# Kernel optimization log

Hardware: AMD Instinct MI355X
Metric: run time of the kernel (lower is better)

The kernel has to match this reference:

```python
import jax, jax.numpy as jnp
import numpy as np

S, N, MSA_DIM, PAIR_DIM, D, H = 8, 256, 256, 128, 32, 8
EPS = 1e-5


def layer_norm(x, w, b):
    mu = jnp.mean(x, axis=-1, keepdims=True)
    var = jnp.mean((x - mu) ** 2, axis=-1, keepdims=True)
    return (x - mu) * jax.lax.rsqrt(var + EPS) * w + b


def setup_inputs() -> dict:
    key = jax.random.key(0)
    ks = jax.random.split(key, 8)
    def rnd(k, shape, scale=1.0):
        return jax.random.normal(k, shape, jnp.float32) * scale
    return {
        "msa_rep": rnd(ks[0], (S, N, MSA_DIM)),
        "pair_rep": rnd(ks[1], (N, N, PAIR_DIM)),
        "ln_w": jnp.ones((MSA_DIM,), jnp.float32),
        "ln_b": jnp.zeros((MSA_DIM,), jnp.float32),
        "w_qkv": rnd(ks[2], (MSA_DIM, 3 * H * D), 0.02),
        "ln_pair_w": jnp.ones((PAIR_DIM,), jnp.float32),
        "ln_pair_b": jnp.zeros((PAIR_DIM,), jnp.float32),
        "w_b": rnd(ks[3], (PAIR_DIM, H), 0.02),
        "w_g": rnd(ks[4], (MSA_DIM, H * D), 0.02),
        "w_out": rnd(ks[5], (H * D, MSA_DIM), 0.02),
        "b_out": jnp.zeros((MSA_DIM,), jnp.float32),
    }


def reference(msa_rep, pair_rep, ln_w, ln_b, w_qkv, ln_pair_w, ln_pair_b,
              w_b, w_g, w_out, b_out):
    s, n, _ = msa_rep.shape
    x = layer_norm(msa_rep, ln_w, ln_b)                      # [s, n, msa_dim]
    qkv = x @ w_qkv                                          # [s, n, 3*h*d]
    # chunk(3, dim=-1) then view(..., d, h): d outer, h inner
    q, k, v = [t.reshape(s, n, D, H) for t in jnp.split(qkv, 3, axis=-1)]
    # pair bias: LN + linear -> [n, n, h], broadcast to [1, i, j, 1, h]
    b = layer_norm(pair_rep, ln_pair_w, ln_pair_b) @ w_b     # [n, n, h]
    g = jax.nn.sigmoid(x @ w_g).reshape(s, n, D, H)          # gate [s, n, d, h]
    # NOTE: logits keep the d axis (no contraction): einsum 'sidh,sjdh->sijdh'
    scores = (q[:, :, None, :, :] * k[:, None, :, :, :]) * (D ** -0.5) \
             + b[None, :, :, None, :]                        # [s, i, j, d, h]
    a = jax.nn.softmax(scores, axis=2)                       # softmax over j
    out = g * jnp.einsum('sijdh,sjdh->sidh', a, v)           # [s, n, d, h]
    return out.reshape(s, n, D * H) @ w_out + b_out          # [s, n, msa_dim]
```

## Files before the change

kernel.cpp:

```cpp
#include <hip/hip_runtime.h>
#include <math.h>

#define S_DIM 8
#define N_RES 256
#define MSA_DIM 256
#define PAIR_DIM 128
#define D_DIM 32
#define H_DIM 8
#define M_ROWS (S_DIM * N_RES)
#define QKV_N (3 * H_DIM * D_DIM)
#define HD (H_DIM * D_DIM)
#define XW_N 1024
#define LOG2E 1.4426950408889634f

typedef __attribute__((ext_vector_type(8))) short short8;
typedef __attribute__((ext_vector_type(4))) float floatx4;

#define DPP_ADD(x, ctrl, rmask)                                                \
    x += __int_as_float(__builtin_amdgcn_update_dpp(                           \
        0, __float_as_int(x), (ctrl), (rmask), 0xf, true))

__device__ __forceinline__ float wave_sum63(float x) {
    DPP_ADD(x, 0x111, 0xf);
    DPP_ADD(x, 0x112, 0xf);
    DPP_ADD(x, 0x114, 0xf);
    DPP_ADD(x, 0x118, 0xf);
    DPP_ADD(x, 0x142, 0xa);
    DPP_ADD(x, 0x143, 0xc);
    return x;
}

__device__ __forceinline__ float quad_sum(float x) {
    x += __int_as_float(__builtin_amdgcn_update_dpp(
        0, __float_as_int(x), 0xB1, 0xf, 0xf, true));
    x += __int_as_float(__builtin_amdgcn_update_dpp(
        0, __float_as_int(x), 0x4E, 0xf, 0xf, true));
    return x;
}

__device__ __forceinline__ unsigned short bf16rn(float v) {
    unsigned u = __float_as_uint(v);
    return (unsigned short)((u + 0x7FFF + ((u >> 16) & 1)) >> 16);
}

__global__ __launch_bounds__(256) void prep_kernel(
    const float* __restrict__ pair, const float* __restrict__ lw,
    const float* __restrict__ lb, const float* __restrict__ wb,
    float* __restrict__ b2,
    const float* __restrict__ w_qkv, const float* __restrict__ w_g,
    unsigned short* __restrict__ whiT, unsigned short* __restrict__ wloT,
    const float* __restrict__ w_out,
    unsigned short* __restrict__ wouthiT, unsigned short* __restrict__ woutloT,
    const float* __restrict__ msa, const float* __restrict__ lnw,
    const float* __restrict__ lnb, unsigned short* __restrict__ xhi,
    unsigned short* __restrict__ xlo)
{
    __shared__ __align__(16) float shm[2080];
    int bx = blockIdx.x;
    int t = threadIdx.x;

    if (bx < 1024) {
        float* As = shm;
        float* Spart = shm + 1552;
        float* Qpart = shm + 1816;
        if (t < 128) {
            float lwc = lw[t];
#pragma unroll
            for (int h = 0; h < 8; h++)
                As[t * 12 + h] = lwc * wb[t * 8 + h] * LOG2E;
        }
        __syncthreads();
        {
            int h = t >> 5, seg = t & 31, cbase = seg * 4;
            float sa = 0, sq = 0;
#pragma unroll
            for (int cc = 0; cc < 4; cc++) {
                int c = cbase + cc;
                sa += As[c * 12 + h];
                sq += lb[c] * wb[c * 8 + h];
            }
            Spart[h * 33 + seg] = sa;
            Qpart[h * 33 + seg] = sq * LOG2E;
        }
        __syncthreads();
        if (t < 8) {
            float s = 0, q = 0;
#pragma unroll
            for (int j = 0; j < 32; j++) {
                s += Spart[t * 33 + j];
                q += Qpart[t * 33 + j];
            }
            As[1536 + t] = s;
            As[1544 + t] = q;
        }
        __syncthreads();
        int row = bx * 64 + (t >> 2);
        int q = t & 3;
        const float* in = pair + (size_t)row * PAIR_DIM;
        float4 x4[8];
#pragma unroll
        for (int it = 0; it < 8; it++)
            x4[it] = *(const float4*)&in[it * 16 + q * 4];
        float s = 0, s2 = 0;
        float dot[8] = {};
#pragma unroll
        for (int it = 0; it < 8; it++) {
            float xk[4];
            *(float4*)xk = x4[it];
#pragma unroll
            for (int k = 0; k < 4; k++) {
                int c = it * 16 + q * 4 + k;
                float xv = xk[k];
                s += xv; s2 += xv * xv;
                float4 A0 = *(const float4*)&As[c * 12];
                float4 A1 = *(const float4*)&As[c * 12 + 4];
                dot[0] += xv * A0.x; dot[1] += xv * A0.y;
                dot[2] += xv * A0.z; dot[3] += xv * A0.w;
                dot[4] += xv * A1.x; dot[5] += xv * A1.y;
                dot[6] += xv * A1.z; dot[7] += xv * A1.w;
            }
        }
        s = quad_sum(s);
        s2 = quad_sum(s2);
#pragma unroll
        for (int h = 0; h < 8; h++) dot[h] = quad_sum(dot[h]);
        float mu = s * (1.0f / 128.0f);
        float var = s2 * (1.0f / 128.0f) - mu * mu;
        float rs = rsqrtf(var + 1e-5f);
        int h0 = q * 2;
#pragma unroll
        for (int u = 0; u < 2; u++) {
            int h = h0 + u;
            b2[h * 65536 + row] = rs * (dot[h] - mu * As[1536 + h]) + As[1544 + h];
        }
    } else if (bx < 1152) {
        int id = (bx - 1024) * 256 + t;
        int n = id >> 5, oct = id & 31, k0 = oct * 8;
        const float* src;
        int stride;
        if (n < QKV_N) { src = w_qkv + n; stride = QKV_N; }
        else           { src = w_g + (n - QKV_N); stride = HD; }
        unsigned short h8[8], l8[8];
#pragma unroll
        for (int j = 0; j < 8; j++) {
            float v = src[(size_t)(k0 + j) * stride];
            unsigned short h = bf16rn(v);
            h8[j] = h;
            l8[j] = bf16rn(v - __uint_as_float((unsigned)h << 16));
        }
        *(short8*)&whiT[n * 256 + k0] = *(short8*)h8;
        *(short8*)&wloT[n * 256 + k0] = *(short8*)l8;
    } else if (bx < 1184) {
        int id = (bx - 1152) * 256 + t;
        int n = id >> 5, oct = id & 31, k0 = oct * 8;
        unsigned short h8[8], l8[8];
#pragma unroll
        for (int j = 0; j < 8; j++) {
            int k = k0 + j;
            int wrow = (k & 31) * 8 + (k >> 5);
            float v = w_out[(size_t)wrow * 256 + n];
            unsigned short h = bf16rn(v);
            h8[j] = h;
            l8[j] = bf16rn(v - __uint_as_float((unsigned)h << 16));
        }
        *(short8*)&wouthiT[n * 256 + k0] = *(short8*)h8;
        *(short8*)&woutloT[n * 256 + k0] = *(short8*)l8;
    } else {
        int row = bx - 1184;
        float v = msa[row * MSA_DIM + t];
        float s1 = wave_sum63(v);
        float s2 = wave_sum63(v * v);
        float* r1 = shm;
        float* r2 = shm + 4;
        int wave = t >> 6, lane = t & 63;
        if (lane == 63) { r1[wave] = s1; r2[wave] = s2; }
        __syncthreads();
        float S1 = r1[0] + r1[1] + r1[2] + r1[3];
        float S2 = r2[0] + r2[1] + r2[2] + r2[3];
        float mu = S1 * (1.0f / 256.0f);
        float var = S2 * (1.0f / 256.0f) - mu * mu;
        float rs = rsqrtf(var + 1e-5f);
        float y = (v - mu) * rs * lnw[t] + lnb[t];
        unsigned short h = bf16rn(y);
        xhi[row * 256 + t] = h;
        xlo[row * 256 + t] = bf16rn(y - __uint_as_float((unsigned)h << 16));
    }
}

__global__ __launch_bounds__(256) void xw_mfma_kernel(
    const unsigned short* __restrict__ xhi, const unsigned short* __restrict__ xlo,
    const unsigned short* __restrict__ whiT, const unsigned short* __restrict__ wloT,
    float* __restrict__ q_t, float* __restrict__ k_t,
    float* __restrict__ v_t, float* __restrict__ g_t)
{
    __shared__ unsigned short As[64 * 72];
    __shared__ unsigned short Bs[128 * 72];
    __shared__ float Cs[64 * 132];
    int t = threadIdx.x;
    int n0 = blockIdx.x * 128, m0 = blockIdx.y * 64;
    int w = t >> 6, L = t & 63;
    int wm = (w & 1) * 32, wn = (w >> 1) * 64;
    int l15 = L & 15, l4 = L >> 4;
    int alm = t >> 3, alk = (t & 7) * 8;
    floatx4 acc[2][4];
#pragma unroll
    for (int a = 0; a < 2; a++)
#pragma unroll
        for (int b = 0; b < 4; b++) acc[a][b] = (floatx4){0, 0, 0, 0};

    short8 pa0 = *(const short8*)&xhi[(m0 + alm) * 256 + alk];
    short8 pa1 = *(const short8*)&xhi[(m0 + alm + 32) * 256 + alk];
    short8 pb[4];
#pragma unroll
    for (int j = 0; j < 4; j++) {
        int id = t + 256 * j;
        int bn = id >> 3, bc = (id & 7) * 8;
        pb[j] = *(const short8*)&whiT[(n0 + bn) * 256 + bc];
    }

    for (int r = 0; r < 12; r++) {
        __syncthreads();
        *(short8*)&As[alm * 72 + alk] = pa0;
        *(short8*)&As[(alm + 32) * 72 + alk] = pa1;
#pragma unroll
        for (int j = 0; j < 4; j++) {
            int id = t + 256 * j;
            int bn = id >> 3, bc = (id & 7) * 8;
            *(short8*)&Bs[bn * 72 + bc] = pb[j];
        }
        __syncthreads();
        if (r < 11) {
            int rn = r + 1;
            int seg = rn >> 2, kb = (rn & 3) * 64;
            const unsigned short* An = (seg == 1) ? xlo : xhi;
            const unsigned short* Bn = (seg == 2) ? wloT : whiT;
            pa0 = *(const short8*)&An[(m0 + alm) * 256 + kb + alk];
            pa1 = *(const short8*)&An[(m0 + alm + 32) * 256 + kb + alk];
#pragma unroll
            for (int j = 0; j < 4; j++) {
                int id = t + 256 * j;
                int bn = id >> 3, bc = (id & 7) * 8;
                pb[j] = *(const short8*)&Bn[(n0 + bn) * 256 + kb + bc];
            }
        }
#pragma unroll
        for (int ks = 0; ks < 2; ks++) {
            int ko = ks * 32 + l4 * 8;
            short8 af[2], bf[4];
#pragma unroll
            for (int a = 0; a < 2; a++)
                af[a] = *(short8*)&As[(wm + a * 16 + l15) * 72 + ko];
#pragma unroll
            for (int b = 0; b < 4; b++)
                bf[b] = *(short8*)&Bs[(wn + b * 16 + l15) * 72 + ko];
#pragma unroll
            for (int a = 0; a < 2; a++)
#pragma unroll
                for (int b = 0; b < 4; b++)
                    acc[a][b] = __builtin_amdgcn_mfma_f32_16x16x32_bf16(
                        af[a], bf[b], acc[a][b], 0, 0, 0);
        }
    }
#pragma unroll
    for (int a = 0; a < 2; a++)
#pragma unroll
        for (int b = 0; b < 4; b++) {
            int nl = wn + b * 16 + l15;
#pragma unroll
            for (int rg = 0; rg < 4; rg++) {
                int ml = wm + a * 16 + l4 * 4 + rg;
                Cs[ml * 132 + nl] = acc[a][b][rg];
            }
        }
    __syncthreads();
    int qkv_mode = (n0 < QKV_N);
    int chunk = n0 >> 8;
    int dbase = (n0 & 255) >> 3;
#pragma unroll
    for (int j = 0; j < 8; j++) {
        int id = t + 256 * j;
        int m = id >> 5;
        int h = (id >> 2) & 7;
        int dq = id & 3;
        float vals[4];
#pragma unroll
        for (int jj = 0; jj < 4; jj++)
            vals[jj] = Cs[m * 132 + (dq * 4 + jj) * 8 + h];
        int mm = m0 + m;
        int daddr = dbase + dq * 4;
        if (qkv_mode) {
            float* dst = (chunk == 0) ? q_t : ((chunk == 1) ? k_t : v_t);
            *(float4*)&dst[(size_t)(h * M_ROWS + mm) * D_DIM + daddr] =
                *(float4*)vals;
        } else {
            float4 o;
            o.x = 1.0f / (1.0f + __expf(-vals[0]));
            o.y = 1.0f / (1.0f + __expf(-vals[1]));
            o.z = 1.0f / (1.0f + __expf(-vals[2]));
            o.w = 1.0f / (1.0f + __expf(-vals[3]));
            *(float4*)&g_t[(size_t)(h * M_ROWS + mm) * D_DIM + daddr] = o;
        }
    }
}

__global__ __launch_bounds__(256) void attn_kernel(
    const float* __restrict__ q_t, const float* __restrict__ k_t,
    const float* __restrict__ v_t, const float* __restrict__ g_t,
    const float* __restrict__ b2, unsigned short* __restrict__ ao_hi,
    unsigned short* __restrict__ ao_lo)
{
    __shared__ float k_sh[256][32];
    __shared__ float v_sh[256][32];
    int blk = blockIdx.x;
    int h = blk & 7, s = (blk >> 3) & 7, it = blk >> 6;
    int t = threadIdx.x;
    const float* kb = k_t + (size_t)(h * M_ROWS + s * N_RES) * D_DIM;
    const float* vb = v_t + (size_t)(h * M_ROWS + s * N_RES) * D_DIM;
    for (int idx = t; idx < 2048; idx += 256) {
        ((float4*)k_sh)[idx] = ((const float4*)kb)[idx];
        ((float4*)v_sh)[idx] = ((const float4*)vb)[idx];
    }
    __syncthreads();
    int jp = t & 3, dg = (t >> 2) & 7, li = t >> 5;
    int d0 = dg * 4;
    const float SCL2 = 0.17677669529663687f * LOG2E;
    int ig[4], mrow[4];
    float qs[4][4];
#pragma unroll
    for (int r = 0; r < 4; r++) {
        ig[r] = it * 32 + r * 8 + li;
        mrow[r] = s * N_RES + ig[r];
        float4 q4 = *(const float4*)&q_t[(size_t)(h * M_ROWS + mrow[r]) * D_DIM + d0];
        qs[r][0] = q4.x * SCL2; qs[r][1] = q4.y * SCL2;
        qs[r][2] = q4.z * SCL2; qs[r][3] = q4.w * SCL2;
    }
    float den[4][4] = {}, acc[4][4] = {};
    const float* bbase = b2 + h * 65536;
    for (int js4 = 0; js4 < 16; js4++) {
        float bb[4][4];
#pragma unroll
        for (int r = 0; r < 4; r++)
            *(float4*)&bb[r][0] =
                *(const float4*)&bbase[ig[r] * 256 + jp * 64 + js4 * 4];
#pragma unroll
        for (int u = 0; u < 4; u++) {
            int j = jp * 64 + js4 * 4 + u;
            float ka[4], va[4];
            *(float4*)ka = *(const float4*)&k_sh[j][d0];
            *(float4*)va = *(const float4*)&v_sh[j][d0];
#pragma unroll
            for (int r = 0; r < 4; r++) {
#pragma unroll
                for (int c = 0; c < 4; c++) {
                    float e = __builtin_amdgcn_exp2f(qs[r][c] * ka[c] + bb[r][u]);
                    den[r][c] += e;
                    acc[r][c] += e * va[c];
                }
            }
        }
    }
#pragma unroll
    for (int r = 0; r < 4; r++)
#pragma unroll
        for (int c = 0; c < 4; c++) {
            den[r][c] = quad_sum(den[r][c]);
            acc[r][c] = quad_sum(acc[r][c]);
        }
    if (jp == 0) {
#pragma unroll
        for (int r = 0; r < 4; r++) {
            float4 g4 = *(const float4*)&g_t[(size_t)(h * M_ROWS + mrow[r]) * D_DIM + d0];
            float o[4];
            o[0] = g4.x * acc[r][0] / den[r][0];
            o[1] = g4.y * acc[r][1] / den[r][1];
            o[2] = g4.z * acc[r][2] / den[r][2];
            o[3] = g4.w * acc[r][3] / den[r][3];
            unsigned short hi[4], lo[4];
#pragma unroll
            for (int c = 0; c < 4; c++) {
                hi[c] = bf16rn(o[c]);
                lo[c] = bf16rn(o[c] - __uint_as_float((unsigned)hi[c] << 16));
            }
            size_t base = (size_t)mrow[r] * 256 + h * 32 + d0;
            uint2 ph, pl;
            ph.x = (unsigned)hi[0] | ((unsigned)hi[1] << 16);
            ph.y = (unsigned)hi[2] | ((unsigned)hi[3] << 16);
            pl.x = (unsigned)lo[0] | ((unsigned)lo[1] << 16);
            pl.y = (unsigned)lo[2] | ((unsigned)lo[3] << 16);
            *(uint2*)&ao_hi[base] = ph;
            *(uint2*)&ao_lo[base] = pl;
        }
    }
}

__global__ __launch_bounds__(256) void out_mfma_kernel(
    const unsigned short* __restrict__ ahi, const unsigned short* __restrict__ alo,
    const unsigned short* __restrict__ whi, const unsigned short* __restrict__ wlo,
    const float* __restrict__ bias, float* __restrict__ out)
{
    __shared__ unsigned short As[64 * 72];
    __shared__ unsigned short Bs[128 * 72];
    __shared__ float Cs[64 * 132];
    int t = threadIdx.x;
    int n0 = blockIdx.x * 128, m0 = blockIdx.y * 64;
    int w = t >> 6, L = t & 63;
    int wm = (w & 1) * 32, wn = (w >> 1) * 64;
    int l15 = L & 15, l4 = L >> 4;
    int alm = t >> 3, alk = (t & 7) * 8;
    floatx4 acc[2][4];
#pragma unroll
    for (int a = 0; a < 2; a++)
#pragma unroll
        for (int b = 0; b < 4; b++) acc[a][b] = (floatx4){0, 0, 0, 0};

    short8 pa0 = *(const short8*)&ahi[(m0 + alm) * 256 + alk];
    short8 pa1 = *(const short8*)&ahi[(m0 + alm + 32) * 256 + alk];
    short8 pb[4];
#pragma unroll
    for (int j = 0; j < 4; j++) {
        int id = t + 256 * j;
        int bn = id >> 3, bc = (id & 7) * 8;
        pb[j] = *(const short8*)&whi[(n0 + bn) * 256 + bc];
    }

    for (int r = 0; r < 12; r++) {
        __syncthreads();
        *(short8*)&As[alm * 72 + alk] = pa0;
        *(short8*)&As[(alm + 32) * 72 + alk] = pa1;
#pragma unroll
        for (int j = 0; j < 4; j++) {
            int id = t + 256 * j;
            int bn = id >> 3, bc = (id & 7) * 8;
            *(short8*)&Bs[bn * 72 + bc] = pb[j];
        }
        __syncthreads();
        if (r < 11) {
            int rn = r + 1;
            int seg = rn >> 2, kb = (rn & 3) * 64;
            const unsigned short* An = (seg == 1) ? alo : ahi;
            const unsigned short* Bn = (seg == 2) ? wlo : whi;
            pa0 = *(const short8*)&An[(m0 + alm) * 256 + kb + alk];
            pa1 = *(const short8*)&An[(m0 + alm + 32) * 256 + kb + alk];
#pragma unroll
            for (int j = 0; j < 4; j++) {
                int id = t + 256 * j;
                int bn = id >> 3, bc = (id & 7) * 8;
                pb[j] = *(const short8*)&Bn[(n0 + bn) * 256 + kb + bc];
            }
        }
#pragma unroll
        for (int ks = 0; ks < 2; ks++) {
            int ko = ks * 32 + l4 * 8;
            short8 af[2], bf[4];
#pragma unroll
            for (int a = 0; a < 2; a++)
                af[a] = *(short8*)&As[(wm + a * 16 + l15) * 72 + ko];
#pragma unroll
            for (int b = 0; b < 4; b++)
                bf[b] = *(short8*)&Bs[(wn + b * 16 + l15) * 72 + ko];
#pragma unroll
            for (int a = 0; a < 2; a++)
#pragma unroll
                for (int b = 0; b < 4; b++)
                    acc[a][b] = __builtin_amdgcn_mfma_f32_16x16x32_bf16(
                        af[a], bf[b], acc[a][b], 0, 0, 0);
        }
    }
#pragma unroll
    for (int a = 0; a < 2; a++)
#pragma unroll
        for (int b = 0; b < 4; b++) {
            int nl = wn + b * 16 + l15;
#pragma unroll
            for (int rg = 0; rg < 4; rg++) {
                int ml = wm + a * 16 + l4 * 4 + rg;
                Cs[ml * 132 + nl] = acc[a][b][rg];
            }
        }
    __syncthreads();
#pragma unroll
    for (int j = 0; j < 8; j++) {
        int id = t + 256 * j;
        int m = id >> 5, nc = (id & 31) * 4;
        float4 v = *(float4*)&Cs[m * 132 + nc];
        float4 bb = *(const float4*)&bias[n0 + nc];
        float4 o;
        o.x = v.x + bb.x; o.y = v.y + bb.y;
        o.z = v.z + bb.z; o.w = v.w + bb.w;
        *(float4*)&out[(size_t)(m0 + m) * 256 + n0 + nc] = o;
    }
}

extern "C" void kernel_launch(void* const* d_in, const int* in_sizes, int n_in,
                              void* d_out, int out_size, void* d_ws, size_t ws_size,
                              hipStream_t stream)
{
    const float* msa_rep   = (const float*)d_in[0];
    const float* pair_rep  = (const float*)d_in[1];
    const float* ln_w      = (const float*)d_in[2];
    const float* ln_b      = (const float*)d_in[3];
    const float* w_qkv     = (const float*)d_in[4];
    const float* ln_pair_w = (const float*)d_in[5];
    const float* ln_pair_b = (const float*)d_in[6];
    const float* w_b       = (const float*)d_in[7];
    const float* w_g       = (const float*)d_in[8];
    const float* w_out     = (const float*)d_in[9];
    const float* b_out     = (const float*)d_in[10];
    float* out = (float*)d_out;

    float* ws = (float*)d_ws;
    const size_t CH = 524288;
    float* q_t = ws + 0 * CH;
    float* k_t = ws + 1 * CH;
    float* v_t = ws + 2 * CH;
    float* g_t = ws + 3 * CH;
    float* b2  = ws + 4 * CH;
    unsigned short* ao_hi   = (unsigned short*)(ws + 5 * CH);
    unsigned short* ao_lo   = ao_hi + (size_t)M_ROWS * 256;
    unsigned short* xhi     = (unsigned short*)(ws + 6 * CH);
    unsigned short* xlo     = xhi + (size_t)M_ROWS * 256;
    unsigned short* whiT    = (unsigned short*)(ws + 7 * CH);
    unsigned short* wloT    = whiT + (size_t)XW_N * 256;
    unsigned short* wouthiT = (unsigned short*)(ws + 8 * CH);
    unsigned short* woutloT = wouthiT + 65536;

    prep_kernel<<<3232, 256, 0, stream>>>(
        pair_rep, ln_pair_w, ln_pair_b, w_b, b2,
        w_qkv, w_g, whiT, wloT,
        w_out, wouthiT, woutloT,
        msa_rep, ln_w, ln_b, xhi, xlo);

    xw_mfma_kernel<<<dim3(8, 32), 256, 0, stream>>>(
        xhi, xlo, whiT, wloT, q_t, k_t, v_t, g_t);

    attn_kernel<<<512, 256, 0, stream>>>(q_t, k_t, v_t, g_t, b2, ao_hi, ao_lo);

    out_mfma_kernel<<<dim3(2, 32), 256, 0, stream>>>(
        ao_hi, ao_lo, wouthiT, woutloT, b_out, out);
}
```

Baseline: 144.3 us.

## Move pair-bias LN into a fused mid kernel alongside smaller-tile QKV GEMM

Pair-bias layernorm/projection moves out of the prep kernel into a new mid kernel. There it runs interleaved (2 of every 3 blocks) with the QKV/gate GEMM, now tiled 64x64 so that more blocks cover the GPU. The output GEMM tiles shrink to 32x64 to raise the block count from 64 to 256. Attention K/V shared arrays get a padded stride of 40 to reduce LDS bank conflicts. Smaller tiles reload more operand data, and the mixed-role kernel has to allocate the larger shared-memory footprint for every block.

```diff
diff --git a/kernel.cpp b/kernel.cpp
--- a/kernel.cpp
+++ b/kernel.cpp
@@ -44,9 +44,6 @@
 }
 
 __global__ __launch_bounds__(256) void prep_kernel(
-    const float* __restrict__ pair, const float* __restrict__ lw,
-    const float* __restrict__ lb, const float* __restrict__ wb,
-    float* __restrict__ b2,
     const float* __restrict__ w_qkv, const float* __restrict__ w_g,
     unsigned short* __restrict__ whiT, unsigned short* __restrict__ wloT,
     const float* __restrict__ w_out,
@@ -55,14 +52,83 @@
     const float* __restrict__ lnb, unsigned short* __restrict__ xhi,
     unsigned short* __restrict__ xlo)
 {
-    __shared__ __align__(16) float shm[2080];
+    __shared__ float shm[8];
     int bx = blockIdx.x;
     int t = threadIdx.x;
 
-    if (bx < 1024) {
-        float* As = shm;
-        float* Spart = shm + 1552;
-        float* Qpart = shm + 1816;
+    if (bx < 2048) {
+        int row = bx;
+        float v = msa[row * MSA_DIM + t];
+        float s1 = wave_sum63(v);
+        float s2 = wave_sum63(v * v);
+        float* r1 = shm;
+        float* r2 = shm + 4;
+        int wave = t >> 6, lane = t & 63;
+        if (lane == 63) { r1[wave] = s1; r2[wave] = s2; }
+        __syncthreads();
+        float S1 = r1[0] + r1[1] + r1[2] + r1[3];
+        float S2 = r2[0] + r2[1] + r2[2] + r2[3];
+        float mu = S1 * (1.0f / 256.0f);
+        float var = S2 * (1.0f / 256.0f) - mu * mu;
+        float rs = rsqrtf(var + 1e-5f);
+        float y = (v - mu) * rs * lnw[t] + lnb[t];
+        unsigned short h = bf16rn(y);
+        xhi[row * 256 + t] = h;
+        xlo[row * 256 + t] = bf16rn(y - __uint_as_float((unsigned)h << 16));
+    } else if (bx < 2176) {
+        int id = (bx - 2048) * 256 + t;
+        int n = id >> 5, oct = id & 31, k0 = oct * 8;
+        const float* src;
+        int stride;
+        if (n < QKV_N) { src = w_qkv + n; stride = QKV_N; }
+        else           { src = w_g + (n - QKV_N); stride = HD; }
+        unsigned short h8[8], l8[8];
+#pragma unroll
+        for (int j = 0; j < 8; j++) {
+            float v = src[(size_t)(k0 + j) * stride];
+            unsigned short h = bf16rn(v);
+            h8[j] = h;
+            l8[j] = bf16rn(v - __uint_as_float((unsigned)h << 16));
+        }
+        *(short8*)&whiT[n * 256 + k0] = *(short8*)h8;
+        *(short8*)&wloT[n * 256 + k0] = *(short8*)l8;
+    } else {
+        int id = (bx - 2176) * 256 + t;
+        int n = id >> 5, oct = id & 31, k0 = oct * 8;
+        unsigned short h8[8], l8[8];
+#pragma unroll
+        for (int j = 0; j < 8; j++) {
+            int k = k0 + j;
+            int wrow = (k & 31) * 8 + (k >> 5);
+            float v = w_out[(size_t)wrow * 256 + n];
+            unsigned short h = bf16rn(v);
+            h8[j] = h;
+            l8[j] = bf16rn(v - __uint_as_float((unsigned)h << 16));
+        }
+        *(short8*)&wouthiT[n * 256 + k0] = *(short8*)h8;
+        *(short8*)&woutloT[n * 256 + k0] = *(short8*)l8;
+    }
+}
+
+__global__ __launch_bounds__(256) void mid_kernel(
+    const float* __restrict__ pair, const float* __restrict__ lw,
+    const float* __restrict__ lb, const float* __restrict__ wb,
+    float* __restrict__ b2,
+    const unsigned short* __restrict__ xhi, const unsigned short* __restrict__ xlo,
+    const unsigned short* __restrict__ whiT, const unsigned short* __restrict__ wloT,
+    float* __restrict__ q_t, float* __restrict__ k_t,
+    float* __restrict__ v_t, float* __restrict__ g_t)
+{
+    __shared__ __align__(16) char smem[35840];
+    int bx = blockIdx.x;
+    int t = threadIdx.x;
+    int g3 = bx / 3, r3 = bx - g3 * 3;
+
+    if (r3 != 2) {
+        float* As = (float*)smem;
+        float* Spart = (float*)smem + 1552;
+        float* Qpart = (float*)smem + 1816;
+        int pair_id = g3 * 2 + r3;
         if (t < 128) {
             float lwc = lw[t];
 #pragma unroll
@@ -94,7 +160,7 @@
             As[1544 + t] = q;
         }
         __syncthreads();
-        int row = bx * 64 + (t >> 2);
+        int row = pair_id * 64 + (t >> 2);
         int q = t & 3;
         const float* in = pair + (size_t)row * PAIR_DIM;
         float4 x4[8];
@@ -133,192 +199,136 @@
             int h = h0 + u;
             b2[h * 65536 + row] = rs * (dot[h] - mu * As[1536 + h]) + As[1544 + h];
         }
-    } else if (bx < 1152) {
-        int id = (bx - 1024) * 256 + t;
-        int n = id >> 5, oct = id & 31, k0 = oct * 8;
-        const float* src;
-        int stride;
-        if (n < QKV_N) { src = w_qkv + n; stride = QKV_N; }
-        else           { src = w_g + (n - QKV_N); stride = HD; }
-        unsigned short h8[8], l8[8];
-#pragma unroll
-        for (int j = 0; j < 8; j++) {
-            float v = src[(size_t)(k0 + j) * stride];
-            unsigned short h = bf16rn(v);
-            h8[j] = h;
-            l8[j] = bf16rn(v - __uint_as_float((unsigned)h << 16));
-        }
-        *(short8*)&whiT[n * 256 + k0] = *(short8*)h8;
-        *(short8*)&wloT[n * 256 + k0] = *(short8*)l8;
-    } else if (bx < 1184) {
-        int id = (bx - 1152) * 256 + t;
-        int n = id >> 5, oct = id & 31, k0 = oct * 8;
-        unsigned short h8[8], l8[8];
-#pragma unroll
-        for (int j = 0; j < 8; j++) {
-            int k = k0 + j;
-            int wrow = (k & 31) * 8 + (k >> 5);
-            float v = w_out[(size_t)wrow * 256 + n];
-            unsigned short h = bf16rn(v);
-            h8[j] = h;
-            l8[j] = bf16rn(v - __uint_as_float((unsigned)h << 16));
-        }
-        *(short8*)&wouthiT[n * 256 + k0] = *(short8*)h8;
-        *(short8*)&woutloT[n * 256 + k0] = *(short8*)l8;
     } else {
-        int row = bx - 1184;
-        float v = msa[row * MSA_DIM + t];
-        float s1 = wave_sum63(v);
-        float s2 = wave_sum63(v * v);
-        float* r1 = shm;
-        float* r2 = shm + 4;
-        int wave = t >> 6, lane = t & 63;
-        if (lane == 63) { r1[wave] = s1; r2[wave] = s2; }
-        __syncthreads();
-        float S1 = r1[0] + r1[1] + r1[2] + r1[3];
-        float S2 = r2[0] + r2[1] + r2[2] + r2[3];
-        float mu = S1 * (1.0f / 256.0f);
-        float var = S2 * (1.0f / 256.0f) - mu * mu;
-        float rs = rsqrtf(var + 1e-5f);
-        float y = (v - mu) * rs * lnw[t] + lnb[t];
-        unsigned short h = bf16rn(y);
-        xhi[row * 256 + t] = h;
-        xlo[row * 256 + t] = bf16rn(y - __uint_as_float((unsigned)h << 16));
-    }
-}
-
-__global__ __launch_bounds__(256) void xw_mfma_kernel(
-    const unsigned short* __restrict__ xhi, const unsigned short* __restrict__ xlo,
-    const unsigned short* __restrict__ whiT, const unsigned short* __restrict__ wloT,
-    float* __restrict__ q_t, float* __restrict__ k_t,
-    float* __restrict__ v_t, float* __restrict__ g_t)
-{
-    __shared__ unsigned short As[64 * 72];
-    __shared__ unsigned short Bs[128 * 72];
-    __shared__ float Cs[64 * 132];
-    int t = threadIdx.x;
-    int n0 = blockIdx.x * 128, m0 = blockIdx.y * 64;
-    int w = t >> 6, L = t & 63;
-    int wm = (w & 1) * 32, wn = (w >> 1) * 64;
-    int l15 = L & 15, l4 = L >> 4;
-    int alm = t >> 3, alk = (t & 7) * 8;
-    floatx4 acc[2][4];
-#pragma unroll
-    for (int a = 0; a < 2; a++)
-#pragma unroll
-        for (int b = 0; b < 4; b++) acc[a][b] = (floatx4){0, 0, 0, 0};
-
-    short8 pa0 = *(const short8*)&xhi[(m0 + alm) * 256 + alk];
-    short8 pa1 = *(const short8*)&xhi[(m0 + alm + 32) * 256 + alk];
-    short8 pb[4];
-#pragma unroll
-    for (int j = 0; j < 4; j++) {
-        int id = t + 256 * j;
-        int bn = id >> 3, bc = (id & 7) * 8;
-        pb[j] = *(const short8*)&whiT[(n0 + bn) * 256 + bc];
-    }
-
-    for (int r = 0; r < 12; r++) {
-        __syncthreads();
-        *(short8*)&As[alm * 72 + alk] = pa0;
-        *(short8*)&As[(alm + 32) * 72 + alk] = pa1;
+        unsigned short* As = (unsigned short*)smem;
+        unsigned short* Bs = As + 64 * 72;
+        float* Cs = (float*)(smem + 18432);
+        int gid = g3;
+        int n0 = (gid & 15) * 64, m0 = (gid >> 4) * 64;
+        int w = t >> 6, L = t & 63;
+        int wm = (w & 1) * 32, wn = (w >> 1) * 32;
+        int l15 = L & 15, l4 = L >> 4;
+        int alm = t >> 3, alk = (t & 7) * 8;
+        floatx4 acc[2][2];
+#pragma unroll
+        for (int a = 0; a < 2; a++)
+#pragma unroll
+            for (int b = 0; b < 2; b++) acc[a][b] = (floatx4){0, 0, 0, 0};
+
+        short8 pa0 = *(const short8*)&xhi[(m0 + alm) * 256 + alk];
+        short8 pa1 = *(const short8*)&xhi[(m0 + alm + 32) * 256 + alk];
+        short8 pb[2];
+#pragma unroll
+        for (int j = 0; j < 2; j++) {
+            int id = t + 256 * j;
+            int bn = id >> 3, bc = (id & 7) * 8;
+            pb[j] = *(const short8*)&whiT[(n0 + bn) * 256 + bc];
+        }
+
+        for (int r = 0; r < 12; r++) {
+            __syncthreads();
+            *(short8*)&As[alm * 72 + alk] = pa0;
+            *(short8*)&As[(alm + 32) * 72 + alk] = pa1;
+#pragma unroll
+            for (int j = 0; j < 2; j++) {
+                int id = t + 256 * j;
+                int bn = id >> 3, bc = (id & 7) * 8;
+                *(short8*)&Bs[bn * 72 + bc] = pb[j];
+            }
+            __syncthreads();
+            if (r < 11) {
+                int rn = r + 1;
+                int seg = rn >> 2, kb = (rn & 3) * 64;
+                const unsigned short* An = (seg == 1) ? xlo : xhi;
+                const unsigned short* Bn = (seg == 2) ? wloT : whiT;
+                pa0 = *(const short8*)&An[(m0 + alm) * 256 + kb + alk];
+                pa1 = *(const short8*)&An[(m0 + alm + 32) * 256 + kb + alk];
+#pragma unroll
+                for (int j = 0; j < 2; j++) {
+                    int id = t + 256 * j;
+                    int bn = id >> 3, bc = (id & 7) * 8;
+                    pb[j] = *(const short8*)&Bn[(n0 + bn) * 256 + kb + bc];
+                }
+            }
+#pragma unroll
+            for (int ks = 0; ks < 2; ks++) {
+                int ko = ks * 32 + l4 * 8;
+                short8 af[2], bf[2];
+#pragma unroll
+                for (int a = 0; a < 2; a++)
+                    af[a] = *(short8*)&As[(wm + a * 16 + l15) * 72 + ko];
+#pragma unroll
+                for (int b = 0; b < 2; b++)
+                    bf[b] = *(short8*)&Bs[(wn + b * 16 + l15) * 72 + ko];
+#pragma unroll
+                for (int a = 0; a < 2; a++)
+#pragma unroll
+                    for (int b = 0; b < 2; b++)
+                        acc[a][b] = __builtin_amdgcn_mfma_f32_16x16x32_bf16(
+                            af[a], bf[b], acc[a][b], 0, 0, 0);
+            }
+        }
+#pragma unroll
+        for (int a = 0; a < 2; a++)
+#pragma unroll
+            for (int b = 0; b < 2; b++) {
+                int nl = wn + b * 16 + l15;
+#pragma unroll
+                for (int rg = 0; rg < 4; rg++) {
+                    int ml = wm + a * 16 + l4 * 4 + rg;
+                    Cs[ml * 68 + nl] = acc[a][b][rg];
+                }
+            }
+        __syncthreads();
+        int qkv_mode = (n0 < QKV_N);
+        int chunk = n0 >> 8;
+        int dbase = (n0 & 255) >> 3;
 #pragma unroll
         for (int j = 0; j < 4; j++) {
             int id = t + 256 * j;
-            int bn = id >> 3, bc = (id & 7) * 8;
-            *(short8*)&Bs[bn * 72 + bc] = pb[j];
-        }
-        __syncthreads();
-        if (r < 11) {
-            int rn = r + 1;
-            int seg = rn >> 2, kb = (rn & 3) * 64;
-            const unsigned short* An = (seg == 1) ? xlo : xhi;
-            const unsigned short* Bn = (seg == 2) ? wloT : whiT;
-            pa0 = *(const short8*)&An[(m0 + alm) * 256 + kb + alk];
-            pa1 = *(const short8*)&An[(m0 + alm + 32) * 256 + kb + alk];
-#pragma unroll
-            for (int j = 0; j < 4; j++) {
-                int id = t + 256 * j;
-                int bn = id >> 3, bc = (id & 7) * 8;
-                pb[j] = *(const short8*)&Bn[(n0 + bn) * 256 + kb + bc];
-            }
-        }
-#pragma unroll
-        for (int ks = 0; ks < 2; ks++) {
-            int ko = ks * 32 + l4 * 8;
-            short8 af[2], bf[4];
-#pragma unroll
-            for (int a = 0; a < 2; a++)
-                af[a] = *(short8*)&As[(wm + a * 16 + l15) * 72 + ko];
-#pragma unroll
-            for (int b = 0; b < 4; b++)
-                bf[b] = *(short8*)&Bs[(wn + b * 16 + l15) * 72 + ko];
-#pragma unroll
-            for (int a = 0; a < 2; a++)
-#pragma unroll
-                for (int b = 0; b < 4; b++)
-                    acc[a][b] = __builtin_amdgcn_mfma_f32_16x16x32_bf16(
-                        af[a], bf[b], acc[a][b], 0, 0, 0);
-        }
-    }
-#pragma unroll
-    for (int a = 0; a < 2; a++)
-#pragma unroll
-        for (int b = 0; b < 4; b++) {
-            int nl = wn + b * 16 + l15;
-#pragma unroll
-            for (int rg = 0; rg < 4; rg++) {
-                int ml = wm + a * 16 + l4 * 4 + rg;
-                Cs[ml * 132 + nl] = acc[a][b][rg];
-            }
-        }
-    __syncthreads();
-    int qkv_mode = (n0 < QKV_N);
-    int chunk = n0 >> 8;
-    int dbase = (n0 & 255) >> 3;
-#pragma unroll
-    for (int j = 0; j < 8; j++) {
-        int id = t + 256 * j;
-        int m = id >> 5;
-        int h = (id >> 2) & 7;
-        int dq = id & 3;
-        float vals[4];
-#pragma unroll
-        for (int jj = 0; jj < 4; jj++)
-            vals[jj] = Cs[m * 132 + (dq * 4 + jj) * 8 + h];
-        int mm = m0 + m;
-        int daddr = dbase + dq * 4;
-        if (qkv_mode) {
-            float* dst = (chunk == 0) ? q_t : ((chunk == 1) ? k_t : v_t);
-            *(float4*)&dst[(size_t)(h * M_ROWS + mm) * D_DIM + daddr] =
-                *(float4*)vals;
-        } else {
-            float4 o;
-            o.x = 1.0f / (1.0f + __expf(-vals[0]));
-            o.y = 1.0f / (1.0f + __expf(-vals[1]));
-            o.z = 1.0f / (1.0f + __expf(-vals[2]));
-            o.w = 1.0f / (1.0f + __expf(-vals[3]));
-            *(float4*)&g_t[(size_t)(h * M_ROWS + mm) * D_DIM + daddr] = o;
-        }
-    }
-}
-
+            int m = id >> 4;
+            int h = (id >> 1) & 7;
+            int dq = id & 1;
+            float vals[4];
+#pragma unroll
+            for (int jj = 0; jj < 4; jj++)
+                vals[jj] = Cs[m * 68 + (dq * 4 + jj) * 8 + h];
+            int mm = m0 + m;
+            int daddr = dbase + dq * 4;
+            if (qkv_mode) {
+                float* dst = (chunk == 0) ? q_t : ((chunk == 1) ? k_t : v_t);
+                *(float4*)&dst[(size_t)(h * M_ROWS + mm) * D_DIM + daddr] =
+                    *(float4*)vals;
+            } else {
+                float4 o;
+                o.x = 1.0f / (1.0f + __expf(-vals[0]));
+                o.y = 1.0f / (1.0f + __expf(-vals[1]));
+                o.z = 1.0f / (1.0f + __expf(-vals[2]));
+                o.w = 1.0f / (1.0f + __expf(-vals[3]));
+                *(float4*)&g_t[(size_t)(h * M_ROWS + mm) * D_DIM + daddr] = o;
+            }
+        }
+    }
+}
+
+#define KV_STR 40
 __global__ __launch_bounds__(256) void attn_kernel(
     const float* __restrict__ q_t, const float* __restrict__ k_t,
     const float* __restrict__ v_t, const float* __restrict__ g_t,
     const float* __restrict__ b2, unsigned short* __restrict__ ao_hi,
     unsigned short* __restrict__ ao_lo)
 {
-    __shared__ float k_sh[256][32];
-    __shared__ float v_sh[256][32];
+    __shared__ float k_sh[256 * KV_STR];
+    __shared__ float v_sh[256 * KV_STR];
     int blk = blockIdx.x;
     int h = blk & 7, s = (blk >> 3) & 7, it = blk >> 6;
     int t = threadIdx.x;
     const float* kb = k_t + (size_t)(h * M_ROWS + s * N_RES) * D_DIM;
     const float* vb = v_t + (size_t)(h * M_ROWS + s * N_RES) * D_DIM;
     for (int idx = t; idx < 2048; idx += 256) {
-        ((float4*)k_sh)[idx] = ((const float4*)kb)[idx];
-        ((float4*)v_sh)[idx] = ((const float4*)vb)[idx];
+        int row = idx >> 3, c = (idx & 7) << 2;
+        *(float4*)&k_sh[row * KV_STR + c] = ((const float4*)kb)[idx];
+        *(float4*)&v_sh[row * KV_STR + c] = ((const float4*)vb)[idx];
     }
     __syncthreads();
     int jp = t & 3, dg = (t >> 2) & 7, li = t >> 5;
@@ -346,8 +356,8 @@
         for (int u = 0; u < 4; u++) {
             int j = jp * 64 + js4 * 4 + u;
             float ka[4], va[4];
-            *(float4*)ka = *(const float4*)&k_sh[j][d0];
-            *(float4*)va = *(const float4*)&v_sh[j][d0];
+            *(float4*)ka = *(const float4*)&k_sh[j * KV_STR + d0];
+            *(float4*)va = *(const float4*)&v_sh[j * KV_STR + d0];
 #pragma unroll
             for (int r = 0; r < 4; r++) {
 #pragma unroll
@@ -398,26 +408,23 @@
     const unsigned short* __restrict__ whi, const unsigned short* __restrict__ wlo,
     const float* __restrict__ bias, float* __restrict__ out)
 {
-    __shared__ unsigned short As[64 * 72];
-    __shared__ unsigned short Bs[128 * 72];
-    __shared__ float Cs[64 * 132];
+    __shared__ unsigned short As[32 * 72];
+    __shared__ unsigned short Bs[64 * 72];
+    __shared__ float Cs[32 * 68];
     int t = threadIdx.x;
-    int n0 = blockIdx.x * 128, m0 = blockIdx.y * 64;
+    int n0 = blockIdx.x * 64, m0 = blockIdx.y * 32;
     int w = t >> 6, L = t & 63;
-    int wm = (w & 1) * 32, wn = (w >> 1) * 64;
+    int wm = (w & 1) * 16, wn = (w >> 1) * 32;
     int l15 = L & 15, l4 = L >> 4;
     int alm = t >> 3, alk = (t & 7) * 8;
-    floatx4 acc[2][4];
-#pragma unroll
-    for (int a = 0; a < 2; a++)
-#pragma unroll
-        for (int b = 0; b < 4; b++) acc[a][b] = (floatx4){0, 0, 0, 0};
+    floatx4 acc[2];
+#pragma unroll
+    for (int b = 0; b < 2; b++) acc[b] = (floatx4){0, 0, 0, 0};
 
     short8 pa0 = *(const short8*)&ahi[(m0 + alm) * 256 + alk];
-    short8 pa1 = *(const short8*)&ahi[(m0 + alm + 32) * 256 + alk];
-    short8 pb[4];
-#pragma unroll
-    for (int j = 0; j < 4; j++) {
+    short8 pb[2];
+#pragma unroll
+    for (int j = 0; j < 2; j++) {
         int id = t + 256 * j;
         int bn = id >> 3, bc = (id & 7) * 8;
         pb[j] = *(const short8*)&whi[(n0 + bn) * 256 + bc];
@@ -426,9 +433,8 @@
     for (int r = 0; r < 12; r++) {
         __syncthreads();
         *(short8*)&As[alm * 72 + alk] = pa0;
-        *(short8*)&As[(alm + 32) * 72 + alk] = pa1;
-#pragma unroll
-        for (int j = 0; j < 4; j++) {
+#pragma unroll
+        for (int j = 0; j < 2; j++) {
             int id = t + 256 * j;
             int bn = id >> 3, bc = (id & 7) * 8;
             *(short8*)&Bs[bn * 72 + bc] = pb[j];
@@ -440,9 +446,8 @@
             const unsigned short* An = (seg == 1) ? alo : ahi;
             const unsigned short* Bn = (seg == 2) ? wlo : whi;
             pa0 = *(const short8*)&An[(m0 + alm) * 256 + kb + alk];
-            pa1 = *(const short8*)&An[(m0 + alm + 32) * 256 + kb + alk];
-#pragma unroll
-            for (int j = 0; j < 4; j++) {
+#pragma unroll
+            for (int j = 0; j < 2; j++) {
                 int id = t + 256 * j;
                 int bn = id >> 3, bc = (id & 7) * 8;
                 pb[j] = *(const short8*)&Bn[(n0 + bn) * 256 + kb + bc];
@@ -451,38 +456,32 @@
 #pragma unroll
         for (int ks = 0; ks < 2; ks++) {
             int ko = ks * 32 + l4 * 8;
-            short8 af[2], bf[4];
-#pragma unroll
-            for (int a = 0; a < 2; a++)
-                af[a] = *(short8*)&As[(wm + a * 16 + l15) * 72 + ko];
-#pragma unroll
-            for (int b = 0; b < 4; b++)
+            short8 af, bf[2];
+            af = *(short8*)&As[(wm + l15) * 72 + ko];
+#pragma unroll
+            for (int b = 0; b < 2; b++)
                 bf[b] = *(short8*)&Bs[(wn + b * 16 + l15) * 72 + ko];
 #pragma unroll
-            for (int a = 0; a < 2; a++)
-#pragma unroll
-                for (int b = 0; b < 4; b++)
-                    acc[a][b] = __builtin_amdgcn_mfma_f32_16x16x32_bf16(
-                        af[a], bf[b], acc[a][b], 0, 0, 0);
-        }
-    }
-#pragma unroll
-    for (int a = 0; a < 2; a++)
-#pragma unroll
-        for (int b = 0; b < 4; b++) {
-            int nl = wn + b * 16 + l15;
-#pragma unroll
-            for (int rg = 0; rg < 4; rg++) {
-                int ml = wm + a * 16 + l4 * 4 + rg;
-                Cs[ml * 132 + nl] = acc[a][b][rg];
-            }
-        }
+            for (int b = 0; b < 2; b++)
+                acc[b] = __builtin_amdgcn_mfma_f32_16x16x32_bf16(
+                    af, bf[b], acc[b], 0, 0, 0);
+        }
+    }
+#pragma unroll
+    for (int b = 0; b < 2; b++) {
+        int nl = wn + b * 16 + l15;
+#pragma unroll
+        for (int rg = 0; rg < 4; rg++) {
+            int ml = wm + l4 * 4 + rg;
+            Cs[ml * 68 + nl] = acc[b][rg];
+        }
+    }
     __syncthreads();
 #pragma unroll
-    for (int j = 0; j < 8; j++) {
+    for (int j = 0; j < 2; j++) {
         int id = t + 256 * j;
-        int m = id >> 5, nc = (id & 31) * 4;
-        float4 v = *(float4*)&Cs[m * 132 + nc];
+        int m = id >> 4, nc = (id & 15) * 4;
+        float4 v = *(float4*)&Cs[m * 68 + nc];
         float4 bb = *(const float4*)&bias[n0 + nc];
         float4 o;
         o.x = v.x + bb.x; o.y = v.y + bb.y;
@@ -524,17 +523,17 @@
     unsigned short* wouthiT = (unsigned short*)(ws + 8 * CH);
     unsigned short* woutloT = wouthiT + 65536;
 
-    prep_kernel<<<3232, 256, 0, stream>>>(
-        pair_rep, ln_pair_w, ln_pair_b, w_b, b2,
+    prep_kernel<<<2208, 256, 0, stream>>>(
         w_qkv, w_g, whiT, wloT,
         w_out, wouthiT, woutloT,
         msa_rep, ln_w, ln_b, xhi, xlo);
 
-    xw_mfma_kernel<<<dim3(8, 32), 256, 0, stream>>>(
+    mid_kernel<<<1536, 256, 0, stream>>>(
+        pair_rep, ln_pair_w, ln_pair_b, w_b, b2,
         xhi, xlo, whiT, wloT, q_t, k_t, v_t, g_t);
 
     attn_kernel<<<512, 256, 0, stream>>>(q_t, k_t, v_t, g_t, b2, ao_hi, ao_lo);
 
-    out_mfma_kernel<<<dim3(2, 32), 256, 0, stream>>>(
+    out_mfma_kernel<<<dim3(4, 64), 256, 0, stream>>>(
         ao_hi, ao_lo, wouthiT, woutloT, b_out, out);
 }
```

After: 146.9 us. Within noise of the previous version (+1.8%).
